# Kernel tuning notes

Hardware: AMD Instinct MI355X
Metric: run time of the kernel (lower is better)

Reference implementation:

```python
import jax, jax.numpy as jnp
import numpy as np


def setup_inputs() -> dict:
    key = jax.random.key(0)
    k1, k2, k3, k4 = jax.random.split(key, 4)
    n, C, t, h, w = 1, 256, 8, 64, 64
    heads = 8
    S = t + h + w - 2  # 134 axial positions per query
    attention = jax.random.normal(k1, (n, heads * S, t, h, w), dtype=jnp.float32)
    value = jax.random.normal(k2, (n, C, t, h, w), dtype=jnp.float32)
    conv_w = jax.random.normal(k3, (C, C), dtype=jnp.float32) / np.float32(np.sqrt(C))
    conv_b = jax.random.normal(k4, (C,), dtype=jnp.float32)
    return {"attention": attention, "value": value, "conv_w": conv_w,
            "conv_b": conv_b, "num_heads": heads}


def _grid_attn_map(A, V):
    """Criss-cross axial attention aggregation.
    A: [b, t+h+w-2, t, h, w] per-query weights over the t-axis (t entries,
       self included), h-axis (h-1 entries, self excluded) and w-axis
       (w-1 entries, self excluded).
    V: [b, c, t, h, w]. Returns [b, c, t, h, w].
    """
    b, c, t, h, w = V.shape
    A_t = A[:, :t]                  # [b, t, t, h, w]
    A_h = A[:, t:t + h - 1]         # [b, h-1, t, h, w]
    A_w = A[:, t + h - 1:]          # [b, w-1, t, h, w]

    # t-axis (self included): sum over key frame s
    out = jnp.einsum('bsthw,bcshw->bcthw', A_t, V)

    # h-axis (self excluded): channel j addresses key row p = j + (j >= q).
    # Build dense [h] channel axis with a zero at p == q via a padded gather.
    zpad = jnp.zeros((b, 1, t, h, w), A.dtype)
    A_h_pad = jnp.concatenate([A_h, zpad], axis=1)  # channel h-1 is zero
    p = jnp.arange(h)[:, None]
    q = jnp.arange(h)[None, :]
    inv_h = jnp.where(p < q, p, jnp.where(p == q, h - 1, p - 1))  # [h(p), h(q)]
    A_h_full = jnp.take_along_axis(A_h_pad, inv_h[None, :, None, :, None], axis=1)  # [b,p,t,q,w]
    out = out + jnp.einsum('bptqw,bctpw->bctqw', A_h_full, V)

    # w-axis (self excluded), same trick along w
    A_w_pad = jnp.concatenate([A_w, zpad], axis=1)  # channel w-1 is zero (h==w here OK; recompute pad generally)
    pw = jnp.arange(w)[:, None]
    qw = jnp.arange(w)[None, :]
    inv_w = jnp.where(pw < qw, pw, jnp.where(pw == qw, w - 1, pw - 1))  # [w(p), w(q)]
    A_w_full = jnp.take_along_axis(A_w_pad, inv_w[None, :, None, None, :], axis=1)  # [b,p,t,h,q]
    out = out + jnp.einsum('bpthq,bcthp->bcthq', A_w_full, V)
    return out


def reference(attention, value, conv_w, conv_b, num_heads):
    n, C, t, h, w = value.shape
    S = t + h + w - 2
    # 1x1x1 Conv3d == per-position channel matmul
    pv = jnp.einsum('ncthw,oc->nothw', value, conv_w) + conv_b[None, :, None, None, None]
    pv = pv.reshape(n * num_heads, C // num_heads, t, h, w)
    A = attention.reshape(n * num_heads, S, t, h, w)
    out = _grid_attn_map(A, pv)
    return out.reshape(n, num_heads, C // num_heads, t, h, w)
```

## Files before the change

### kernel.cpp

```cpp
#include <hip/hip_runtime.h>

#define SS   134
#define HWP  4096
#define THW  32768

typedef float f32x4 __attribute__((ext_vector_type(4)));
typedef short bf16x8 __attribute__((ext_vector_type(8)));
typedef short bf16x4 __attribute__((ext_vector_type(4)));

__device__ __forceinline__ unsigned short f2bf(float f) {
  unsigned int u = __float_as_uint(f);
  u += 0x7fff + ((u >> 16) & 1);
  return (unsigned short)(u >> 16);
}

__global__ __launch_bounds__(256) void conv1x1_v2(
    const float* __restrict__ V, const float* __restrict__ W,
    const float* __restrict__ bias, float* __restrict__ PV) {
  __shared__ unsigned short sW[256 * 40];
  __shared__ unsigned short sV[32 * 40];
  const int tid = threadIdx.x;
  const int x0 = blockIdx.x * 32;
  const int lane = tid & 63;
  const int wv = tid >> 6;
  const int m = lane & 15;
  const int q = lane >> 4;

  f32x4 acc[4][2];
#pragma unroll
  for (int i = 0; i < 4; ++i)
#pragma unroll
    for (int j = 0; j < 2; ++j)
      acc[i][j] = (f32x4){0.f, 0.f, 0.f, 0.f};

  for (int k0 = 0; k0 < 256; k0 += 32) {
#pragma unroll 2
    for (int r = 0; r < 8; ++r) {
      const int f = r * 256 + tid;
      const int o = f >> 3;
      const int c4 = (f & 7) * 4;
      const float4 w4 = *(const float4*)&W[o * 256 + k0 + c4];
      bf16x4 b;
      b.x = (short)f2bf(w4.x);
      b.y = (short)f2bf(w4.y);
      b.z = (short)f2bf(w4.z);
      b.w = (short)f2bf(w4.w);
      *(bf16x4*)&sW[o * 40 + c4] = b;
    }
    {
      const int c = tid >> 3;
      const int x4 = (tid & 7) * 4;
      const float4 v4 = *(const float4*)&V[(size_t)(k0 + c) * THW + x0 + x4];
      sV[(x4 + 0) * 40 + c] = f2bf(v4.x);
      sV[(x4 + 1) * 40 + c] = f2bf(v4.y);
      sV[(x4 + 2) * 40 + c] = f2bf(v4.z);
      sV[(x4 + 3) * 40 + c] = f2bf(v4.w);
    }
    __syncthreads();
    bf16x8 fa[4], fb[2];
#pragma unroll
    for (int i = 0; i < 4; ++i)
      fa[i] = *(const bf16x8*)&sW[(wv * 64 + i * 16 + m) * 40 + q * 8];
#pragma unroll
    for (int j = 0; j < 2; ++j)
      fb[j] = *(const bf16x8*)&sV[(j * 16 + m) * 40 + q * 8];
#pragma unroll
    for (int i = 0; i < 4; ++i)
#pragma unroll
      for (int j = 0; j < 2; ++j)
        acc[i][j] = __builtin_amdgcn_mfma_f32_16x16x32_bf16(fa[i], fb[j], acc[i][j], 0, 0, 0);
    __syncthreads();
  }

#pragma unroll
  for (int i = 0; i < 4; ++i) {
#pragma unroll
    for (int r = 0; r < 4; ++r) {
      const int o = wv * 64 + i * 16 + q * 4 + r;
      const float b = bias[o];
#pragma unroll
      for (int j = 0; j < 2; ++j)
        PV[(size_t)o * THW + x0 + j * 16 + m] = acc[i][j][r] + b;
    }
  }
}

__global__ __launch_bounds__(512) void attn_th(
    const float* __restrict__ A, const float* __restrict__ PV,
    float* __restrict__ O) {
  const int b = blockIdx.x;
  const int hd = b & 7;
  const int qb = (b >> 3) & 3;
  const int tq = b >> 5;
  const int tid = threadIdx.x;
  const int lane = tid & 63;
  const int wv = tid >> 6;
  const int w4 = (lane & 15) * 4;
  const int cl = lane >> 4;
  const int ch = wv & 1;
  const int qg = wv >> 1;
  const int q0 = qb * 16 + qg * 4;

  __shared__ float slab[2][8 * 32 * 64];

  const float* __restrict__ Ab = A + (size_t)hd * SS * THW + (size_t)tq * HWP;
  const size_t pvh = (size_t)hd * 32 * THW;
  const float* __restrict__ PVh = PV + pvh;

  f32x4 acc[4][4];
#pragma unroll
  for (int i = 0; i < 4; ++i)
#pragma unroll
    for (int j = 0; j < 4; ++j)
      acc[i][j] = (f32x4){0.f, 0.f, 0.f, 0.f};

  const int c_s = tid >> 4;
  const int w4s = (tid & 15) * 4;
  const float* __restrict__ pvstage =
      PVh + (size_t)c_s * THW + (size_t)tq * HWP + w4s;
  const int sbase = c_s * 64 + w4s;

  f32x4 stg[8];
#pragma unroll
  for (int r = 0; r < 8; ++r) stg[r] = *(const f32x4*)&pvstage[r * 64];

  for (int s = 0; s < 8; ++s) {
#pragma unroll
    for (int qi = 0; qi < 4; ++qi) {
      const int q = q0 + qi;
      const f32x4 a = *(const f32x4*)&Ab[(size_t)s * THW + q * 64 + w4];
#pragma unroll
      for (int g = 0; g < 4; ++g) {
        const int c = ch * 16 + g * 4 + cl;
        const f32x4 v =
            *(const f32x4*)&PVh[(size_t)c * THW + (size_t)s * HWP + q * 64 + w4];
        acc[qi][g] += a * v;
      }
    }
  }

#pragma unroll
  for (int r = 0; r < 8; ++r)
    *(f32x4*)&slab[0][r * 2048 + sbase] = stg[r];
  __syncthreads();

  for (int ck = 0; ck < 8; ++ck) {
    const int cur = ck & 1;
    if (ck < 7) {
#pragma unroll
      for (int r = 0; r < 8; ++r)
        stg[r] = *(const f32x4*)&pvstage[((ck + 1) * 8 + r) * 64];
    }
#pragma unroll
    for (int pp = 0; pp < 8; ++pp) {
      const int p = ck * 8 + pp;
      f32x4 a[4];
#pragma unroll
      for (int qi = 0; qi < 4; ++qi) {
        const int q = q0 + qi;
        const int row = p - (q < p ? 1 : 0);
        f32x4 av = *(const f32x4*)&Ab[(size_t)(8 + row) * THW + q * 64 + w4];
        if (q == p) av = (f32x4){0.f, 0.f, 0.f, 0.f};
        a[qi] = av;
      }
      f32x4 v[4];
#pragma unroll
      for (int g = 0; g < 4; ++g)
        v[g] = *(const f32x4*)&slab[cur][pp * 2048 + (ch * 16 + g * 4 + cl) * 64 + w4];
#pragma unroll
      for (int qi = 0; qi < 4; ++qi)
#pragma unroll
        for (int g = 0; g < 4; ++g)
          acc[qi][g] += a[qi] * v[g];
    }
    __syncthreads();
    if (ck < 7) {
#pragma unroll
      for (int r = 0; r < 8; ++r)
        *(f32x4*)&slab[cur ^ 1][r * 2048 + sbase] = stg[r];
      __syncthreads();
    }
  }

#pragma unroll
  for (int qi = 0; qi < 4; ++qi) {
    const int q = q0 + qi;
#pragma unroll
    for (int g = 0; g < 4; ++g) {
      const int c = ch * 16 + g * 4 + cl;
      *(f32x4*)&O[pvh + (size_t)c * THW + (size_t)tq * HWP + q * 64 + w4] =
          acc[qi][g];
    }
  }
}

__global__ __launch_bounds__(256) void attn_w(
    const float* __restrict__ A, const float* __restrict__ PV,
    float* __restrict__ O) {
  const int b = blockIdx.x;
  const int hb = b & 15;
  const int tq = (b >> 4) & 7;
  const int hd = b >> 7;
  const int tid = threadIdx.x;
  const int wq = tid & 63;
  const int cg = tid >> 6;
  const int h0 = hb * 4;

  __shared__ float slab[32 * 64 * 4];

  const float* __restrict__ Ab = A + (size_t)hd * SS * THW + (size_t)tq * HWP;
  const size_t pvh = (size_t)hd * 32 * THW;

#pragma unroll 4
  for (int i = 0; i < 8; ++i) {
    const int fid = tid + i * 256;
    const int w4s = (fid & 15) * 4;
    const int h = (fid >> 4) & 3;
    const int c = fid >> 6;
    const f32x4 v =
        *(const f32x4*)&PV[pvh + (size_t)c * THW + (size_t)tq * HWP + (h0 + h) * 64 + w4s];
    slab[(c * 64 + w4s + 0) * 4 + h] = v.x;
    slab[(c * 64 + w4s + 1) * 4 + h] = v.y;
    slab[(c * 64 + w4s + 2) * 4 + h] = v.z;
    slab[(c * 64 + w4s + 3) * 4 + h] = v.w;
  }

  f32x4 racc[8];
#pragma unroll
  for (int ci = 0; ci < 8; ++ci) {
    const int c = cg + ci * 4;
    f32x4 r;
#pragma unroll
    for (int hh = 0; hh < 4; ++hh)
      r[hh] = O[pvh + (size_t)c * THW + (size_t)tq * HWP + (h0 + hh) * 64 + wq];
    racc[ci] = r;
  }
  __syncthreads();

#pragma unroll 2
  for (int p = 0; p < 64; ++p) {
    const int row = 71 + p - (wq <= p ? 1 : 0);
    const float* pa = Ab + (size_t)row * THW + h0 * 64 + wq;
    f32x4 a;
    a.x = pa[0];
    a.y = pa[64];
    a.z = pa[128];
    a.w = pa[192];
    if (p == wq) a = (f32x4){0.f, 0.f, 0.f, 0.f};
#pragma unroll
    for (int ci = 0; ci < 8; ++ci) {
      const f32x4 v = *(const f32x4*)&slab[(cg + ci * 4) * 256 + p * 4];
      racc[ci] += a * v;
    }
  }

#pragma unroll
  for (int ci = 0; ci < 8; ++ci) {
    const int c = cg + ci * 4;
#pragma unroll
    for (int hh = 0; hh < 4; ++hh)
      O[pvh + (size_t)c * THW + (size_t)tq * HWP + (h0 + hh) * 64 + wq] = racc[ci][hh];
  }
}

extern "C" void kernel_launch(void* const* d_in, const int* in_sizes, int n_in,
                              void* d_out, int out_size, void* d_ws, size_t ws_size,
                              hipStream_t stream) {
  const float* A = (const float*)d_in[0];
  const float* V = (const float*)d_in[1];
  const float* W = (const float*)d_in[2];
  const float* bias = (const float*)d_in[3];
  float* out = (float*)d_out;
  float* pv = (float*)d_ws;

  conv1x1_v2<<<dim3(1024), 256, 0, stream>>>(V, W, bias, pv);
  attn_th<<<dim3(256), 512, 0, stream>>>(A, pv, out);
  attn_w<<<dim3(1024), 256, 0, stream>>>(A, pv, out);
}
```

Measured before the change: 347.7 us.

## Pre-convert conv weights to bf16 and double attn_th threads per block

Adds a small kernel that converts the 1x1 conv weights to bf16 once, writing them into the output buffer as scratch, so each conv block loads ready bf16 weight tiles instead of converting fp32 per block. attn_th now uses 1024 threads per block, with each wave handling 2 query rows instead of 4 and staging work split across twice as many threads, to raise parallelism and cut per-thread registers. The trade-off is an extra launch and the use of the output buffer as temporary storage before it is overwritten.

```diff
diff --git a/kernel.cpp b/kernel.cpp
--- a/kernel.cpp
+++ b/kernel.cpp
@@ -14,8 +14,20 @@
   return (unsigned short)(u >> 16);
 }
 
-__global__ __launch_bounds__(256) void conv1x1_v2(
-    const float* __restrict__ V, const float* __restrict__ W,
+__global__ __launch_bounds__(256) void w2bf(const float* __restrict__ W,
+                                            unsigned short* __restrict__ Wbf) {
+  const int i = (blockIdx.x * 256 + threadIdx.x) * 4;
+  const float4 w4 = *(const float4*)&W[i];
+  bf16x4 b;
+  b.x = (short)f2bf(w4.x);
+  b.y = (short)f2bf(w4.y);
+  b.z = (short)f2bf(w4.z);
+  b.w = (short)f2bf(w4.w);
+  *(bf16x4*)&Wbf[i] = b;
+}
+
+__global__ __launch_bounds__(256) void conv1x1_v3(
+    const float* __restrict__ V, const unsigned short* __restrict__ Wbf,
     const float* __restrict__ bias, float* __restrict__ PV) {
   __shared__ unsigned short sW[256 * 40];
   __shared__ unsigned short sV[32 * 40];
@@ -34,18 +46,12 @@
       acc[i][j] = (f32x4){0.f, 0.f, 0.f, 0.f};
 
   for (int k0 = 0; k0 < 256; k0 += 32) {
-#pragma unroll 2
-    for (int r = 0; r < 8; ++r) {
-      const int f = r * 256 + tid;
-      const int o = f >> 3;
-      const int c4 = (f & 7) * 4;
-      const float4 w4 = *(const float4*)&W[o * 256 + k0 + c4];
-      bf16x4 b;
-      b.x = (short)f2bf(w4.x);
-      b.y = (short)f2bf(w4.y);
-      b.z = (short)f2bf(w4.z);
-      b.w = (short)f2bf(w4.w);
-      *(bf16x4*)&sW[o * 40 + c4] = b;
+#pragma unroll
+    for (int r = 0; r < 4; ++r) {
+      const int s8 = r * 256 + tid;
+      const int o = s8 >> 2;
+      const int c8 = (s8 & 3) * 8;
+      *(bf16x8*)&sW[o * 40 + c8] = *(const bf16x8*)&Wbf[o * 256 + k0 + c8];
     }
     {
       const int c = tid >> 3;
@@ -85,7 +91,7 @@
   }
 }
 
-__global__ __launch_bounds__(512) void attn_th(
+__global__ __launch_bounds__(1024, 4) void attn_th(
     const float* __restrict__ A, const float* __restrict__ PV,
     float* __restrict__ O) {
   const int b = blockIdx.x;
@@ -99,7 +105,7 @@
   const int cl = lane >> 4;
   const int ch = wv & 1;
   const int qg = wv >> 1;
-  const int q0 = qb * 16 + qg * 4;
+  const int q0 = qb * 16 + qg * 2;
 
   __shared__ float slab[2][8 * 32 * 64];
 
@@ -107,26 +113,28 @@
   const size_t pvh = (size_t)hd * 32 * THW;
   const float* __restrict__ PVh = PV + pvh;
 
-  f32x4 acc[4][4];
-#pragma unroll
-  for (int i = 0; i < 4; ++i)
+  f32x4 acc[2][4];
+#pragma unroll
+  for (int i = 0; i < 2; ++i)
 #pragma unroll
     for (int j = 0; j < 4; ++j)
       acc[i][j] = (f32x4){0.f, 0.f, 0.f, 0.f};
 
-  const int c_s = tid >> 4;
+  const int c_s = (tid >> 4) & 31;
   const int w4s = (tid & 15) * 4;
+  const int pp0 = tid >> 9;
   const float* __restrict__ pvstage =
       PVh + (size_t)c_s * THW + (size_t)tq * HWP + w4s;
   const int sbase = c_s * 64 + w4s;
 
-  f32x4 stg[8];
-#pragma unroll
-  for (int r = 0; r < 8; ++r) stg[r] = *(const f32x4*)&pvstage[r * 64];
+  f32x4 stg[4];
+#pragma unroll
+  for (int r = 0; r < 4; ++r)
+    stg[r] = *(const f32x4*)&pvstage[(pp0 + 2 * r) * 64];
 
   for (int s = 0; s < 8; ++s) {
 #pragma unroll
-    for (int qi = 0; qi < 4; ++qi) {
+    for (int qi = 0; qi < 2; ++qi) {
       const int q = q0 + qi;
       const f32x4 a = *(const f32x4*)&Ab[(size_t)s * THW + q * 64 + w4];
 #pragma unroll
@@ -140,23 +148,23 @@
   }
 
 #pragma unroll
-  for (int r = 0; r < 8; ++r)
-    *(f32x4*)&slab[0][r * 2048 + sbase] = stg[r];
+  for (int r = 0; r < 4; ++r)
+    *(f32x4*)&slab[0][(pp0 + 2 * r) * 2048 + sbase] = stg[r];
   __syncthreads();
 
   for (int ck = 0; ck < 8; ++ck) {
     const int cur = ck & 1;
     if (ck < 7) {
 #pragma unroll
-      for (int r = 0; r < 8; ++r)
-        stg[r] = *(const f32x4*)&pvstage[((ck + 1) * 8 + r) * 64];
+      for (int r = 0; r < 4; ++r)
+        stg[r] = *(const f32x4*)&pvstage[((ck + 1) * 8 + pp0 + 2 * r) * 64];
     }
 #pragma unroll
     for (int pp = 0; pp < 8; ++pp) {
       const int p = ck * 8 + pp;
-      f32x4 a[4];
-#pragma unroll
-      for (int qi = 0; qi < 4; ++qi) {
+      f32x4 a[2];
+#pragma unroll
+      for (int qi = 0; qi < 2; ++qi) {
         const int q = q0 + qi;
         const int row = p - (q < p ? 1 : 0);
         f32x4 av = *(const f32x4*)&Ab[(size_t)(8 + row) * THW + q * 64 + w4];
@@ -168,7 +176,7 @@
       for (int g = 0; g < 4; ++g)
         v[g] = *(const f32x4*)&slab[cur][pp * 2048 + (ch * 16 + g * 4 + cl) * 64 + w4];
 #pragma unroll
-      for (int qi = 0; qi < 4; ++qi)
+      for (int qi = 0; qi < 2; ++qi)
 #pragma unroll
         for (int g = 0; g < 4; ++g)
           acc[qi][g] += a[qi] * v[g];
@@ -176,14 +184,14 @@
     __syncthreads();
     if (ck < 7) {
 #pragma unroll
-      for (int r = 0; r < 8; ++r)
-        *(f32x4*)&slab[cur ^ 1][r * 2048 + sbase] = stg[r];
+      for (int r = 0; r < 4; ++r)
+        *(f32x4*)&slab[cur ^ 1][(pp0 + 2 * r) * 2048 + sbase] = stg[r];
       __syncthreads();
     }
   }
 
 #pragma unroll
-  for (int qi = 0; qi < 4; ++qi) {
+  for (int qi = 0; qi < 2; ++qi) {
     const int q = q0 + qi;
 #pragma unroll
     for (int g = 0; g < 4; ++g) {
@@ -273,7 +281,10 @@
   float* out = (float*)d_out;
   float* pv = (float*)d_ws;
 
-  conv1x1_v2<<<dim3(1024), 256, 0, stream>>>(V, W, bias, pv);
-  attn_th<<<dim3(256), 512, 0, stream>>>(A, pv, out);
+  unsigned short* Wbf = (unsigned short*)d_out;
+
+  w2bf<<<dim3(64), 256, 0, stream>>>(W, Wbf);
+  conv1x1_v3<<<dim3(1024), 256, 0, stream>>>(V, Wbf, bias, pv);
+  attn_th<<<dim3(256), 1024, 0, stream>>>(A, pv, out);
   attn_w<<<dim3(1024), 256, 0, stream>>>(A, pv, out);
 }
```

New measurement: 360.6 us. 3.7% more time.

## Split t-axis aggregation into own kernel and pre-convert conv weights to bf16

Applied to the files above, without the earlier changes.

Weights are converted to bf16 once in a small pre-kernel that writes into the output buffer as scratch, so the conv kernel loads bf16 directly instead of converting fp32 in every block. The t-axis aggregation moves out of the h-axis kernel into a separate kernel, parallelised over 512 blocks. That kernel reuses each PV load across all 8 query frames, and the h kernel now starts from the partial output it reads back. This raises parallelism for the t-axis work and removes redundant weight conversion, at the cost of extra launches and an extra read/write of the output.

```diff
diff --git a/kernel.cpp b/kernel.cpp
--- a/kernel.cpp
+++ b/kernel.cpp
@@ -14,8 +14,20 @@
   return (unsigned short)(u >> 16);
 }
 
-__global__ __launch_bounds__(256) void conv1x1_v2(
-    const float* __restrict__ V, const float* __restrict__ W,
+__global__ __launch_bounds__(256) void w2bf(const float* __restrict__ W,
+                                            unsigned short* __restrict__ Wbf) {
+  const int i = (blockIdx.x * 256 + threadIdx.x) * 4;
+  const float4 w4 = *(const float4*)&W[i];
+  bf16x4 b;
+  b.x = (short)f2bf(w4.x);
+  b.y = (short)f2bf(w4.y);
+  b.z = (short)f2bf(w4.z);
+  b.w = (short)f2bf(w4.w);
+  *(bf16x4*)&Wbf[i] = b;
+}
+
+__global__ __launch_bounds__(256) void conv1x1_v3(
+    const float* __restrict__ V, const unsigned short* __restrict__ Wbf,
     const float* __restrict__ bias, float* __restrict__ PV) {
   __shared__ unsigned short sW[256 * 40];
   __shared__ unsigned short sV[32 * 40];
@@ -34,18 +46,12 @@
       acc[i][j] = (f32x4){0.f, 0.f, 0.f, 0.f};
 
   for (int k0 = 0; k0 < 256; k0 += 32) {
-#pragma unroll 2
-    for (int r = 0; r < 8; ++r) {
-      const int f = r * 256 + tid;
-      const int o = f >> 3;
-      const int c4 = (f & 7) * 4;
-      const float4 w4 = *(const float4*)&W[o * 256 + k0 + c4];
-      bf16x4 b;
-      b.x = (short)f2bf(w4.x);
-      b.y = (short)f2bf(w4.y);
-      b.z = (short)f2bf(w4.z);
-      b.w = (short)f2bf(w4.w);
-      *(bf16x4*)&sW[o * 40 + c4] = b;
+#pragma unroll
+    for (int r = 0; r < 4; ++r) {
+      const int s8 = r * 256 + tid;
+      const int o = s8 >> 2;
+      const int c8 = (s8 & 3) * 8;
+      *(bf16x8*)&sW[o * 40 + c8] = *(const bf16x8*)&Wbf[o * 256 + k0 + c8];
     }
     {
       const int c = tid >> 3;
@@ -85,7 +91,53 @@
   }
 }
 
-__global__ __launch_bounds__(512) void attn_th(
+__global__ __launch_bounds__(256) void attn_t(
+    const float* __restrict__ A, const float* __restrict__ PV,
+    float* __restrict__ O) {
+  const int b = blockIdx.x;
+  const int hd = b & 7;
+  const int cb = (b >> 3) & 3;
+  const int xt = b >> 5;
+  const int tid = threadIdx.x;
+  const int xi = xt * 256 + (tid & 63) * 4;
+  const int cq = tid >> 6;
+
+  const float* __restrict__ At = A + (size_t)hd * SS * THW + xi;
+  const size_t pvh = (size_t)hd * 32 * THW;
+
+  f32x4 acc[8][2];
+#pragma unroll
+  for (int t = 0; t < 8; ++t)
+#pragma unroll
+    for (int ci = 0; ci < 2; ++ci)
+      acc[t][ci] = (f32x4){0.f, 0.f, 0.f, 0.f};
+
+  for (int s = 0; s < 8; ++s) {
+    f32x4 pvv[2];
+#pragma unroll
+    for (int ci = 0; ci < 2; ++ci) {
+      const int c = cb * 8 + cq * 2 + ci;
+      pvv[ci] = *(const f32x4*)&PV[pvh + (size_t)c * THW + (size_t)s * HWP + xi];
+    }
+#pragma unroll
+    for (int t = 0; t < 8; ++t) {
+      const f32x4 a = *(const f32x4*)&At[(size_t)s * THW + (size_t)t * HWP];
+#pragma unroll
+      for (int ci = 0; ci < 2; ++ci)
+        acc[t][ci] += a * pvv[ci];
+    }
+  }
+
+#pragma unroll
+  for (int t = 0; t < 8; ++t)
+#pragma unroll
+    for (int ci = 0; ci < 2; ++ci) {
+      const int c = cb * 8 + cq * 2 + ci;
+      *(f32x4*)&O[pvh + (size_t)c * THW + (size_t)t * HWP + xi] = acc[t][ci];
+    }
+}
+
+__global__ __launch_bounds__(512) void attn_h(
     const float* __restrict__ A, const float* __restrict__ PV,
     float* __restrict__ O) {
   const int b = blockIdx.x;
@@ -109,10 +161,15 @@
 
   f32x4 acc[4][4];
 #pragma unroll
-  for (int i = 0; i < 4; ++i)
-#pragma unroll
-    for (int j = 0; j < 4; ++j)
-      acc[i][j] = (f32x4){0.f, 0.f, 0.f, 0.f};
+  for (int qi = 0; qi < 4; ++qi) {
+    const int q = q0 + qi;
+#pragma unroll
+    for (int g = 0; g < 4; ++g) {
+      const int c = ch * 16 + g * 4 + cl;
+      acc[qi][g] =
+          *(const f32x4*)&O[pvh + (size_t)c * THW + (size_t)tq * HWP + q * 64 + w4];
+    }
+  }
 
   const int c_s = tid >> 4;
   const int w4s = (tid & 15) * 4;
@@ -123,22 +180,6 @@
   f32x4 stg[8];
 #pragma unroll
   for (int r = 0; r < 8; ++r) stg[r] = *(const f32x4*)&pvstage[r * 64];
-
-  for (int s = 0; s < 8; ++s) {
-#pragma unroll
-    for (int qi = 0; qi < 4; ++qi) {
-      const int q = q0 + qi;
-      const f32x4 a = *(const f32x4*)&Ab[(size_t)s * THW + q * 64 + w4];
-#pragma unroll
-      for (int g = 0; g < 4; ++g) {
-        const int c = ch * 16 + g * 4 + cl;
-        const f32x4 v =
-            *(const f32x4*)&PVh[(size_t)c * THW + (size_t)s * HWP + q * 64 + w4];
-        acc[qi][g] += a * v;
-      }
-    }
-  }
-
 #pragma unroll
   for (int r = 0; r < 8; ++r)
     *(f32x4*)&slab[0][r * 2048 + sbase] = stg[r];
@@ -166,7 +207,7 @@
       f32x4 v[4];
 #pragma unroll
       for (int g = 0; g < 4; ++g)
-        v[g] = *(const f32x4*)&slab[cur][pp * 2048 + (ch * 16 + g * 4 + cl) * 64 + w4];
+        v[g] = *(const f32x4*)&slab[cur][pp * 2048 + (g * 4 + cl + ch * 16) * 64 + w4];
 #pragma unroll
       for (int qi = 0; qi < 4; ++qi)
 #pragma unroll
@@ -273,7 +314,11 @@
   float* out = (float*)d_out;
   float* pv = (float*)d_ws;
 
-  conv1x1_v2<<<dim3(1024), 256, 0, stream>>>(V, W, bias, pv);
-  attn_th<<<dim3(256), 512, 0, stream>>>(A, pv, out);
+  unsigned short* Wbf = (unsigned short*)d_out;
+
+  w2bf<<<dim3(64), 256, 0, stream>>>(W, Wbf);
+  conv1x1_v3<<<dim3(1024), 256, 0, stream>>>(V, Wbf, bias, pv);
+  attn_t<<<dim3(512), 256, 0, stream>>>(A, pv, out);
+  attn_h<<<dim3(256), 512, 0, stream>>>(A, pv, out);
   attn_w<<<dim3(1024), 256, 0, stream>>>(A, pv, out);
 }
```

Result: slower. 370.4 us (+6.5%).
